# Performance work log

Measured on AMD Instinct MI355X. Metric: run time of the kernel, lower is better.

Reference implementation:

```python
import jax, jax.numpy as jnp
import numpy as np

B, L, D = 4, 4096, 256


def setup_inputs() -> dict:
    key = jax.random.key(0)
    k_x, k_q, k_k, k_v, k_w, k_b = jax.random.split(key, 6)
    s = 1.0 / np.sqrt(D)
    return {
        "x": jax.random.normal(k_x, (B, L, D), dtype=jnp.float32),
        "Wq": jax.random.normal(k_q, (D, D), dtype=jnp.float32) * s,   # nn.Linear weight (out,in)
        "Wk": jax.random.normal(k_k, (D, D), dtype=jnp.float32) * s,
        "Wv": jax.random.normal(k_v, (D, D), dtype=jnp.float32) * s,
        "w_mlp": jax.random.normal(k_w, (D,), dtype=jnp.float32) * s,  # Linear(D,1) weight
        "b_mlp": jnp.zeros((), dtype=jnp.float32),                     # Linear(D,1) bias
    }


def reference(x, Wq, Wk, Wv, w_mlp, b_mlp):
    # Projections (nn.Linear: y = x @ W.T, no bias)
    Q = jnp.einsum("bld,ed->ble", x, Wq)
    K = jnp.einsum("bld,ed->ble", x, Wk)
    V = jnp.einsum("bld,ed->ble", x, Wv)
    # score[b,i,j] = relu((Q[b,i]-K[b,j]) @ w_mlp + b_mlp)
    # decomposed: (Q-K)@w = Q@w - K@w  (exact same math, no (B,L,L,D) tensor)
    q_s = Q @ w_mlp  # (B,L)
    k_s = K @ w_mlp  # (B,L)
    scores = jax.nn.relu(q_s[:, :, None] - k_s[:, None, :] + b_mlp)  # (B,L,L)
    attn = jax.nn.softmax(scores, axis=-1)  # softmax over key axis j
    # out[b,i,d] = sum_j attn[b,i,j] * V[b,j,d]
    out = jnp.einsum("bij,bjd->bid", attn, V)
    return out  # dropout p=0.0 is identity
```

## Files before the change

kernel.cpp:

```cpp
#include <hip/hip_runtime.h>
#include <math.h>

#define BB 4
#define LL 4096
#define DD 256
#define NROWS (BB*LL)
#define CHUNK 32
#define NC (LL/CHUNK)
#define NB 8192

typedef __bf16 bf16x8 __attribute__((ext_vector_type(8)));
typedef __bf16 bf16x4 __attribute__((ext_vector_type(4)));
typedef float floatx4 __attribute__((ext_vector_type(4)));

__global__ void k_prep(const float* __restrict__ Wq, const float* __restrict__ Wk,
                       const float* __restrict__ Wv, const float* __restrict__ w,
                       float* __restrict__ u_part,
                       __bf16* __restrict__ Wh, __bf16* __restrict__ Wl) {
    __shared__ float wl[16];
    int d = threadIdx.x;
    int e0 = blockIdx.x * 16;
    if (d < 16) wl[d] = w[e0 + d];
    __syncthreads();
    float aq = 0.f, ak = 0.f;
    #pragma unroll
    for (int j = 0; j < 16; ++j) {
        float we = wl[j];
        aq = fmaf(Wq[(size_t)(e0 + j)*DD + d], we, aq);
        ak = fmaf(Wk[(size_t)(e0 + j)*DD + d], we, ak);
        float wv = Wv[(size_t)(e0 + j)*DD + d];
        __bf16 h = (__bf16)wv;
        Wh[(size_t)(e0 + j)*DD + d] = h;
        Wl[(size_t)(e0 + j)*DD + d] = (__bf16)(wv - (float)h);
    }
    u_part[(size_t)blockIdx.x*512 + d]       = aq;
    u_part[(size_t)blockIdx.x*512 + DD + d]  = ak;
}

__global__ void __launch_bounds__(256) k_gemm_mfma(
        const float* __restrict__ x,
        const __bf16* __restrict__ Wh, const __bf16* __restrict__ Wl,
        const float* __restrict__ u_part, const float* __restrict__ bmlp,
        float* __restrict__ V, float* __restrict__ a, float* __restrict__ c) {
    __shared__ __bf16 Ah[2][32*40];
    __shared__ __bf16 Al[2][32*40];
    __shared__ float4 ul[128];
    __shared__ float pros[512];
    const int tid = threadIdx.x;
    const int wave = tid >> 6, lane = tid & 63;
    const int rowBase = blockIdx.x * 32;
    const int colBase = blockIdx.y * 128;
    const int quad = lane >> 4, l16 = lane & 15;
    const int srow = tid >> 3, skq = (tid & 7) * 4;
    const bool doproj = (blockIdx.y == 0);

    if (doproj && tid < 128) {
        float4 s = make_float4(0.f, 0.f, 0.f, 0.f);
        #pragma unroll
        for (int g = 0; g < 16; ++g) {
            float4 p = *(const float4*)(u_part + (size_t)g*512 + tid*4);
            s.x += p.x; s.y += p.y; s.z += p.z; s.w += p.w;
        }
        ul[tid] = s;
    }
    __syncthreads();

    floatx4 acc[2][2];
    #pragma unroll
    for (int rt = 0; rt < 2; ++rt)
        #pragma unroll
        for (int ct = 0; ct < 2; ++ct)
            acc[rt][ct] = (floatx4){0.f, 0.f, 0.f, 0.f};
    float aq = 0.f, ak = 0.f;

    const float* xrow = x + (size_t)(rowBase + srow)*DD + skq;

    {
        float4 xv = *(const float4*)xrow;
        __bf16 h0 = (__bf16)xv.x, h1 = (__bf16)xv.y, h2 = (__bf16)xv.z, h3 = (__bf16)xv.w;
        bf16x4 hv = {h0, h1, h2, h3};
        bf16x4 lv = {(__bf16)(xv.x - (float)h0), (__bf16)(xv.y - (float)h1),
                     (__bf16)(xv.z - (float)h2), (__bf16)(xv.w - (float)h3)};
        *(bf16x4*)&Ah[0][srow*40 + skq] = hv;
        *(bf16x4*)&Al[0][srow*40 + skq] = lv;
        if (doproj) {
            float4 q4 = ul[(tid & 7)];
            float4 k4 = ul[64 + (tid & 7)];
            aq = fmaf(xv.x, q4.x, fmaf(xv.y, q4.y, fmaf(xv.z, q4.z, fmaf(xv.w, q4.w, aq))));
            ak = fmaf(xv.x, k4.x, fmaf(xv.y, k4.y, fmaf(xv.z, k4.z, fmaf(xv.w, k4.w, ak))));
        }
    }
    __syncthreads();

    for (int t = 0; t < 8; ++t) {
        const int k0 = t * 32;
        const int cur = t & 1;
        float4 xv;
        if (t < 7) xv = *(const float4*)(xrow + k0 + 32);
        bf16x8 ah[2], al[2];
        #pragma unroll
        for (int rt = 0; rt < 2; ++rt) {
            int m = rt*16 + l16;
            ah[rt] = *(bf16x8*)&Ah[cur][m*40 + quad*8];
            al[rt] = *(bf16x8*)&Al[cur][m*40 + quad*8];
        }
        if (t < 7) {
            __bf16 h0 = (__bf16)xv.x, h1 = (__bf16)xv.y, h2 = (__bf16)xv.z, h3 = (__bf16)xv.w;
            bf16x4 hv = {h0, h1, h2, h3};
            bf16x4 lv = {(__bf16)(xv.x - (float)h0), (__bf16)(xv.y - (float)h1),
                         (__bf16)(xv.z - (float)h2), (__bf16)(xv.w - (float)h3)};
            *(bf16x4*)&Ah[cur^1][srow*40 + skq] = hv;
            *(bf16x4*)&Al[cur^1][srow*40 + skq] = lv;
            if (doproj) {
                float4 q4 = ul[((k0 + 32) >> 2) + (tid & 7)];
                float4 k4 = ul[64 + ((k0 + 32) >> 2) + (tid & 7)];
                aq = fmaf(xv.x, q4.x, fmaf(xv.y, q4.y, fmaf(xv.z, q4.z, fmaf(xv.w, q4.w, aq))));
                ak = fmaf(xv.x, k4.x, fmaf(xv.y, k4.y, fmaf(xv.z, k4.z, fmaf(xv.w, k4.w, ak))));
            }
        }
        __syncthreads();
        #pragma unroll
        for (int ct = 0; ct < 2; ++ct) {
            int n = colBase + wave*32 + ct*16 + l16;
            bf16x8 bh = *(const bf16x8*)(Wh + (size_t)n*DD + k0 + quad*8);
            bf16x8 bl = *(const bf16x8*)(Wl + (size_t)n*DD + k0 + quad*8);
            #pragma unroll
            for (int rt = 0; rt < 2; ++rt) {
                acc[rt][ct] = __builtin_amdgcn_mfma_f32_16x16x32_bf16(ah[rt], bh, acc[rt][ct], 0, 0, 0);
                acc[rt][ct] = __builtin_amdgcn_mfma_f32_16x16x32_bf16(ah[rt], bl, acc[rt][ct], 0, 0, 0);
                acc[rt][ct] = __builtin_amdgcn_mfma_f32_16x16x32_bf16(al[rt], bh, acc[rt][ct], 0, 0, 0);
            }
        }
    }
    #pragma unroll
    for (int rt = 0; rt < 2; ++rt)
        #pragma unroll
        for (int ct = 0; ct < 2; ++ct)
            #pragma unroll
            for (int i = 0; i < 4; ++i) {
                int row = rowBase + rt*16 + quad*4 + i;
                int col = colBase + wave*32 + ct*16 + l16;
                V[(size_t)row*DD + col] = acc[rt][ct][i];
            }
    if (doproj) {
        __syncthreads();
        pros[tid] = aq;
        pros[256 + tid] = ak;
        __syncthreads();
        if (tid < 32) {
            float sa = 0.f, sc = 0.f;
            #pragma unroll
            for (int j = 0; j < 8; ++j) {
                sa += pros[tid*8 + j];
                sc += pros[256 + tid*8 + j];
            }
            a[rowBase + tid] = sa + bmlp[0];
            c[rowBase + tid] = sc;
        }
    }
}

__global__ void __launch_bounds__(1024) k_sortish(const float* __restrict__ c,
        const float* __restrict__ a,
        int* __restrict__ perm,
        float* __restrict__ c_sorted, float* __restrict__ e_sorted,
        float* __restrict__ SE, float* __restrict__ hdr,
        float4* __restrict__ rowrec, int* __restrict__ rbs_g) {
    __shared__ int   hist[NB];
    __shared__ float esl[LL];
    __shared__ float scrf[64];
    __shared__ int   qhist[132];
    __shared__ int   rbs[132];
    int b = blockIdx.x, tid = threadIdx.x;
    int wave = tid >> 6, lane = tid & 63;
    int* scri = (int*)scrf;

    float4 cv = ((const float4*)(c + (size_t)b*LL))[tid];
    float cw[4] = {cv.x, cv.y, cv.z, cv.w};
    float mn = fminf(fminf(cw[0],cw[1]), fminf(cw[2],cw[3]));
    float mx = fmaxf(fmaxf(cw[0],cw[1]), fmaxf(cw[2],cw[3]));
    #pragma unroll
    for (int off = 32; off > 0; off >>= 1) {
        mn = fminf(mn, __shfl_down(mn, off));
        mx = fmaxf(mx, __shfl_down(mx, off));
    }
    if (lane == 0) { scrf[wave] = mn; scrf[32 + wave] = mx; }
    __syncthreads();
    if (wave == 0) {
        float m = (lane < 16) ? scrf[lane]      :  3.4e38f;
        float M = (lane < 16) ? scrf[32 + lane] : -3.4e38f;
        #pragma unroll
        for (int off = 32; off > 0; off >>= 1) {
            m = fminf(m, __shfl_down(m, off));
            M = fmaxf(M, __shfl_down(M, off));
        }
        if (lane == 0) { scrf[0] = m; scrf[1] = M; }
    }
    __syncthreads();
    float cmin = scrf[0], cmax = scrf[1];
    float scale = (float)NB / fmaxf(cmax - cmin, 1e-20f);
    __syncthreads();

    ((int4*)hist)[tid] = make_int4(0,0,0,0);
    ((int4*)hist)[tid + 1024] = make_int4(0,0,0,0);
    if (tid < 132) qhist[tid] = 0;
    __syncthreads();

    int bins[4];
    #pragma unroll
    for (int u = 0; u < 4; ++u) {
        int bi = (int)((cw[u] - cmin) * scale);
        bi = bi < 0 ? 0 : (bi > NB-1 ? NB-1 : bi);
        bins[u] = bi;
        atomicAdd(&hist[bi], 1);
    }
    __syncthreads();

    int loc[8]; int base = 0;
    #pragma unroll
    for (int j = 0; j < 8; ++j) { loc[j] = base; base += hist[tid*8 + j]; }
    int incl = base;
    #pragma unroll
    for (int off = 1; off < 64; off <<= 1) {
        int t = __shfl_up(incl, off);
        if (lane >= off) incl += t;
    }
    if (lane == 63) scri[wave] = incl;
    __syncthreads();
    if (wave == 0) {
        int v = (lane < 16) ? scri[lane] : 0;
        int s = v;
        #pragma unroll
        for (int off = 1; off < 16; off <<= 1) {
            int t = __shfl_up(s, off);
            if (lane >= off) s += t;
        }
        if (lane < 16) scri[lane] = s - v;
    }
    __syncthreads();
    int thread_excl = (incl - base) + scri[wave];
    __syncthreads();
    #pragma unroll
    for (int j = 0; j < 8; ++j) {
        int bs = thread_excl + loc[j];
        hist[tid*8 + j] = bs;
    }
    if (tid == 0) {
        hdr[b*2 + 0] = cmin;
        hdr[b*2 + 1] = scale;
    }
    __syncthreads();

    float4 av = ((const float4*)(a + (size_t)b*LL))[tid];
    float aw[4] = {av.x, av.y, av.z, av.w};
    int qq[4]; float4 rec[4];
    #pragma unroll
    for (int u = 0; u < 4; ++u) {
        float t = (aw[u] - cmin) * scale;
        int ibb = t < 0.f ? 0 : (t >= (float)NB ? NB : (int)t);
        int k   = (ibb == NB)     ? LL : hist[ibb];
        int ke  = (ibb >= NB - 1) ? LL : hist[ibb + 1];
        qq[u] = k >> 5;
        rec[u] = make_float4(aw[u], __int_as_float(k), __int_as_float(ke),
                             __int_as_float(tid*4 + u));
        atomicAdd(&qhist[qq[u]], 1);
    }
    __syncthreads();

    #pragma unroll
    for (int u = 0; u < 4; ++u) {
        int i = tid*4 + u;
        int r = atomicAdd(&hist[bins[u]], 1);
        float e = expf(cmin - cw[u]);
        perm[(size_t)b*LL + r] = i;
        c_sorted[(size_t)b*LL + r] = cw[u];
        e_sorted[(size_t)b*LL + r] = e;
        esl[r] = e;
    }
    __syncthreads();

    if (wave == 0) {
        int v0 = qhist[2*lane], v1 = qhist[2*lane+1];
        int ps = v0 + v1;
        int qi = ps;
        #pragma unroll
        for (int off = 1; off < 64; off <<= 1) {
            int tu = __shfl_up(qi, off);
            if (lane >= off) qi += tu;
        }
        rbs[2*lane]     = qi - ps;
        rbs[2*lane + 1] = qi - v1;
        if (lane == 63) { rbs[128] = qi; rbs[129] = qi + qhist[128]; }
    }
    __syncthreads();
    if (tid < 129) qhist[tid] = rbs[tid];
    if (tid < 130) rbs_g[b*130 + tid] = rbs[tid];
    __syncthreads();
    #pragma unroll
    for (int u = 0; u < 4; ++u) {
        int r = atomicAdd(&qhist[qq[u]], 1);
        rowrec[(size_t)b*LL + r] = rec[u];
    }

    float le[4]; float s0 = 0.f;
    #pragma unroll
    for (int u = 0; u < 4; ++u) { le[u] = s0; s0 += esl[tid*4 + u]; }
    float fincl = s0;
    #pragma unroll
    for (int off = 1; off < 64; off <<= 1) {
        float t = __shfl_up(fincl, off);
        if (lane >= off) fincl += t;
    }
    if (lane == 63) scrf[wave] = fincl;
    __syncthreads();
    if (wave == 0) {
        float v = (lane < 16) ? scrf[lane] : 0.f;
        float s = v;
        #pragma unroll
        for (int off = 1; off < 16; off <<= 1) {
            float t = __shfl_up(s, off);
            if (lane >= off) s += t;
        }
        if (lane < 16) scrf[lane] = s - v;
    }
    __syncthreads();
    float texcl = (fincl - s0) + scrf[wave];
    #pragma unroll
    for (int u = 0; u < 4; ++u)
        SE[(size_t)b*(LL+1) + tid*4 + u] = texcl + le[u];
    if (tid == 1023) SE[(size_t)b*(LL+1) + LL] = texcl + s0;
}

__device__ __forceinline__ void chunk_out_phase(
    int b, int q, int tid, const float (&vr)[CHUNK], const float* ev_l,
    float* Plds, float* Pelds,
    float* bp_l, float* be_l, float* pt_l, float* pe_l,
    const float* __restrict__ baseP, const float* __restrict__ basePe,
    const float4* __restrict__ rowrec, const int* __restrict__ rbs_g,
    const float* __restrict__ SE, const float* __restrict__ hdr,
    const float* __restrict__ c_sorted, const float* __restrict__ e_sorted,
    const int* __restrict__ perm, const float* __restrict__ V,
    float* __restrict__ out)
{
    {
        size_t o  = ((size_t)b*(NC+1) + q)*DD + tid;
        size_t ot = ((size_t)b*(NC+1) + NC)*DD + tid;
        bp_l[tid] = baseP[o];  be_l[tid] = basePe[o];
        pt_l[tid] = baseP[ot]; pe_l[tid] = basePe[ot];
    }
    float accp = 0.f, acce = 0.f;
    #pragma unroll
    for (int r = 0; r < CHUNK; ++r) {
        Plds[r*DD + tid] = accp; Pelds[r*DD + tid] = acce;
        accp += vr[r]; acce = fmaf(ev_l[r], vr[r], acce);
    }
    Plds[CHUNK*DD + tid] = accp; Pelds[CHUNK*DD + tid] = acce;
    __syncthreads();
    const int wave = tid >> 6, lane = tid & 63;
    const int db = lane * 4;
    const float cmin = hdr[b*2];
    const float4 bp4 = *(const float4*)&bp_l[db];
    const float4 be4 = *(const float4*)&be_l[db];
    const float4 pt4 = *(const float4*)&pt_l[db];
    const int rs = rbs_g[b*130 + q];
    const int re = rbs_g[b*130 + q + ((q == NC-1) ? 2 : 1)];
    for (int t = rs + wave; t < re; t += 4) {
        float4 rr = rowrec[(size_t)b*LL + t];
        float ai = rr.x;
        int k    = __float_as_int(rr.y);
        int kend = __float_as_int(rr.z);
        int i    = __float_as_int(rr.w);
        float alpha = expf(cmin - ai);
        int local = k - q*CHUNK;
        const float4 pl4 = *(const float4*)&Plds[local*DD + db];
        const float4 pe4 = *(const float4*)&Pelds[local*DD + db];
        float Z = fmaf(alpha, (float)(LL - k), SE[(size_t)b*(LL+1) + k]);
        float4 num;
        num.x = fmaf(alpha, pt4.x - (pl4.x + bp4.x), pe4.x + be4.x);
        num.y = fmaf(alpha, pt4.y - (pl4.y + bp4.y), pe4.y + be4.y);
        num.z = fmaf(alpha, pt4.z - (pl4.z + bp4.z), pe4.z + be4.z);
        num.w = fmaf(alpha, pt4.w - (pl4.w + bp4.w), pe4.w + be4.w);
        for (int r = k; r < kend; ++r) {
            float cr = c_sorted[(size_t)b*LL + r];
            if (cr < ai) {
                float w = e_sorted[(size_t)b*LL + r] - alpha;
                int j = perm[(size_t)b*LL + r];
                float4 v = *(const float4*)(V + ((size_t)b*LL + j)*DD + db);
                num.x = fmaf(w, v.x, num.x);
                num.y = fmaf(w, v.y, num.y);
                num.z = fmaf(w, v.z, num.z);
                num.w = fmaf(w, v.w, num.w);
                Z += w;
            }
        }
        float invZ = 1.f / Z;
        float4 o;
        o.x = num.x * invZ; o.y = num.y * invZ; o.z = num.z * invZ; o.w = num.w * invZ;
        *(float4*)(out + ((size_t)b*LL + i)*DD + db) = o;
    }
}

__global__ void __launch_bounds__(256) k_tot(
    const float* __restrict__ V, const int* __restrict__ perm,
    const float* __restrict__ e_sorted,
    float* __restrict__ Tp, float* __restrict__ Te)
{
    __shared__ float ev_l[CHUNK];
    __shared__ int   pj_l[CHUNK];
    const int q = blockIdx.x, b = blockIdx.y, tid = threadIdx.x;
    if (tid < CHUNK) {
        pj_l[tid] = perm[(size_t)b*LL + q*CHUNK + tid];
        ev_l[tid] = e_sorted[(size_t)b*LL + q*CHUNK + tid];
    }
    __syncthreads();
    float sp = 0.f, se = 0.f;
    #pragma unroll
    for (int r = 0; r < CHUNK; ++r) {
        float v = V[((size_t)b*LL + pj_l[r])*DD + tid];
        sp += v; se = fmaf(ev_l[r], v, se);
    }
    Tp[((size_t)b*NC + q)*DD + tid] = sp;
    Te[((size_t)b*NC + q)*DD + tid] = se;
}

__global__ void k_base(const float* __restrict__ Tp, const float* __restrict__ Te,
        float* __restrict__ baseP, float* __restrict__ basePe) {
    int q = blockIdx.x, b = blockIdx.y, d = threadIdx.x;
    float acc = 0.f, acce = 0.f;
    #pragma unroll 8
    for (int i = 0; i < q; ++i) {
        size_t ti = ((size_t)b*NC + i) * DD + d;
        acc += Tp[ti]; acce += Te[ti];
    }
    size_t o = ((size_t)b*(NC+1) + q) * DD + d;
    baseP[o] = acc; basePe[o] = acce;
}

__global__ void __launch_bounds__(256, 2) k_outf(
    const float* __restrict__ V, const int* __restrict__ perm,
    const float* __restrict__ e_sorted, const float* __restrict__ c_sorted,
    const float4* __restrict__ rowrec, const int* __restrict__ rbs_g,
    const float* __restrict__ SE, const float* __restrict__ hdr,
    const float* __restrict__ baseP, const float* __restrict__ basePe,
    float* __restrict__ out)
{
    __shared__ float Plds[(CHUNK+1)*DD];
    __shared__ float Pelds[(CHUNK+1)*DD];
    __shared__ float bp_l[DD], be_l[DD], pt_l[DD], pe_l[DD];
    __shared__ float ev_l[CHUNK];
    __shared__ int   pj_l[CHUNK];
    const int q = blockIdx.x, b = blockIdx.y, tid = threadIdx.x;
    if (tid < CHUNK) {
        pj_l[tid] = perm[(size_t)b*LL + q*CHUNK + tid];
        ev_l[tid] = e_sorted[(size_t)b*LL + q*CHUNK + tid];
    }
    __syncthreads();
    float vr[CHUNK];
    #pragma unroll
    for (int r = 0; r < CHUNK; ++r)
        vr[r] = V[((size_t)b*LL + pj_l[r])*DD + tid];
    chunk_out_phase(b, q, tid, vr, ev_l, Plds, Pelds, bp_l, be_l, pt_l, pe_l,
                    baseP, basePe, rowrec, rbs_g, SE, hdr,
                    c_sorted, e_sorted, perm, V, out);
}

extern "C" void kernel_launch(void* const* d_in, const int* in_sizes, int n_in,
                              void* d_out, int out_size, void* d_ws, size_t ws_size,
                              hipStream_t stream) {
    const float* x  = (const float*)d_in[0];
    const float* Wq = (const float*)d_in[1];
    const float* Wk = (const float*)d_in[2];
    const float* Wv = (const float*)d_in[3];
    const float* wm = (const float*)d_in[4];
    const float* bm = (const float*)d_in[5];
    float* out = (float*)d_out;
    float* ws = (float*)d_ws;

    size_t off = 0;
    auto alloc = [&](size_t n) {
        float* p = ws + off;
        off += (n + 255) & ~(size_t)255;
        return p;
    };
    float* u_part   = alloc(16*512);
    float* a        = alloc(NROWS);
    float* c        = alloc(NROWS);
    float* c_sorted = alloc(NROWS);
    float* e_sorted = alloc(NROWS);
    float* SE       = alloc((size_t)BB*(LL+1));
    int*   perm     = (int*)alloc(NROWS);
    float* hdr      = alloc(2*BB);
    float* V        = alloc((size_t)NROWS*DD);
    float* Tp       = alloc((size_t)BB*NC*DD);
    float* Te       = alloc((size_t)BB*NC*DD);
    float* baseP    = alloc((size_t)BB*(NC+1)*DD);
    float* basePe   = alloc((size_t)BB*(NC+1)*DD);
    float4* rowrec  = (float4*)alloc((size_t)NROWS*4);
    int*   rbs_g    = (int*)alloc(BB*130);
    __bf16* Wh      = (__bf16*)alloc((size_t)DD*DD/2);
    __bf16* Wl      = (__bf16*)alloc((size_t)DD*DD/2);

    hipLaunchKernelGGL(k_prep, dim3(16), dim3(DD), 0, stream, Wq, Wk, Wv, wm, u_part, Wh, Wl);
    hipLaunchKernelGGL(k_gemm_mfma, dim3(NROWS/32, 2), dim3(256), 0, stream,
                       x, Wh, Wl, u_part, bm, V, a, c);
    hipLaunchKernelGGL(k_sortish, dim3(BB), dim3(1024), 0, stream,
                       c, a, perm, c_sorted, e_sorted, SE, hdr, rowrec, rbs_g);
    hipLaunchKernelGGL(k_tot, dim3(NC, BB), dim3(256), 0, stream,
                       V, perm, e_sorted, Tp, Te);
    hipLaunchKernelGGL(k_base, dim3(NC+1, BB), dim3(256), 0, stream,
                       Tp, Te, baseP, basePe);
    hipLaunchKernelGGL(k_outf, dim3(NC, BB), dim3(256), 0, stream,
                       V, perm, e_sorted, c_sorted, rowrec, rbs_g,
                       SE, hdr, baseP, basePe, out);
}
```

Measured before the change: 140.9 us.

## Widen GEMM tile to full D and fold chunk-prefix kernel into output kernel

The GEMM kernel now computes all 256 output columns per 32-row block instead of splitting columns across two blocks. This halves the grid, removes the duplicated x loads and bf16 split work, and lets every block compute the a/c projections. The separate k_base prefix-sum kernel is removed. k_outf instead sums the per-chunk totals Tp/Te itself to get its exclusive prefix and the grand total, which drops one launch and the baseP/basePe round trip. The cost is more accumulator registers in the GEMM, less parallelism there, and each output block reading all NC chunk totals.

```diff
diff --git a/kernel.cpp b/kernel.cpp
--- a/kernel.cpp
+++ b/kernel.cpp
@@ -49,12 +49,10 @@
     const int tid = threadIdx.x;
     const int wave = tid >> 6, lane = tid & 63;
     const int rowBase = blockIdx.x * 32;
-    const int colBase = blockIdx.y * 128;
     const int quad = lane >> 4, l16 = lane & 15;
     const int srow = tid >> 3, skq = (tid & 7) * 4;
-    const bool doproj = (blockIdx.y == 0);
-
-    if (doproj && tid < 128) {
+
+    if (tid < 128) {
         float4 s = make_float4(0.f, 0.f, 0.f, 0.f);
         #pragma unroll
         for (int g = 0; g < 16; ++g) {
@@ -65,11 +63,11 @@
     }
     __syncthreads();
 
-    floatx4 acc[2][2];
+    floatx4 acc[2][4];
     #pragma unroll
     for (int rt = 0; rt < 2; ++rt)
         #pragma unroll
-        for (int ct = 0; ct < 2; ++ct)
+        for (int ct = 0; ct < 4; ++ct)
             acc[rt][ct] = (floatx4){0.f, 0.f, 0.f, 0.f};
     float aq = 0.f, ak = 0.f;
 
@@ -83,12 +81,10 @@
                      (__bf16)(xv.z - (float)h2), (__bf16)(xv.w - (float)h3)};
         *(bf16x4*)&Ah[0][srow*40 + skq] = hv;
         *(bf16x4*)&Al[0][srow*40 + skq] = lv;
-        if (doproj) {
-            float4 q4 = ul[(tid & 7)];
-            float4 k4 = ul[64 + (tid & 7)];
-            aq = fmaf(xv.x, q4.x, fmaf(xv.y, q4.y, fmaf(xv.z, q4.z, fmaf(xv.w, q4.w, aq))));
-            ak = fmaf(xv.x, k4.x, fmaf(xv.y, k4.y, fmaf(xv.z, k4.z, fmaf(xv.w, k4.w, ak))));
-        }
+        float4 q4 = ul[(tid & 7)];
+        float4 k4 = ul[64 + (tid & 7)];
+        aq = fmaf(xv.x, q4.x, fmaf(xv.y, q4.y, fmaf(xv.z, q4.z, fmaf(xv.w, q4.w, aq))));
+        ak = fmaf(xv.x, k4.x, fmaf(xv.y, k4.y, fmaf(xv.z, k4.z, fmaf(xv.w, k4.w, ak))));
     }
     __syncthreads();
 
@@ -111,17 +107,15 @@
                          (__bf16)(xv.z - (float)h2), (__bf16)(xv.w - (float)h3)};
             *(bf16x4*)&Ah[cur^1][srow*40 + skq] = hv;
             *(bf16x4*)&Al[cur^1][srow*40 + skq] = lv;
-            if (doproj) {
-                float4 q4 = ul[((k0 + 32) >> 2) + (tid & 7)];
-                float4 k4 = ul[64 + ((k0 + 32) >> 2) + (tid & 7)];
-                aq = fmaf(xv.x, q4.x, fmaf(xv.y, q4.y, fmaf(xv.z, q4.z, fmaf(xv.w, q4.w, aq))));
-                ak = fmaf(xv.x, k4.x, fmaf(xv.y, k4.y, fmaf(xv.z, k4.z, fmaf(xv.w, k4.w, ak))));
-            }
+            float4 q4 = ul[((k0 + 32) >> 2) + (tid & 7)];
+            float4 k4 = ul[64 + ((k0 + 32) >> 2) + (tid & 7)];
+            aq = fmaf(xv.x, q4.x, fmaf(xv.y, q4.y, fmaf(xv.z, q4.z, fmaf(xv.w, q4.w, aq))));
+            ak = fmaf(xv.x, k4.x, fmaf(xv.y, k4.y, fmaf(xv.z, k4.z, fmaf(xv.w, k4.w, ak))));
         }
         __syncthreads();
         #pragma unroll
-        for (int ct = 0; ct < 2; ++ct) {
-            int n = colBase + wave*32 + ct*16 + l16;
+        for (int ct = 0; ct < 4; ++ct) {
+            int n = wave*64 + ct*16 + l16;
             bf16x8 bh = *(const bf16x8*)(Wh + (size_t)n*DD + k0 + quad*8);
             bf16x8 bl = *(const bf16x8*)(Wl + (size_t)n*DD + k0 + quad*8);
             #pragma unroll
@@ -135,14 +129,14 @@
     #pragma unroll
     for (int rt = 0; rt < 2; ++rt)
         #pragma unroll
-        for (int ct = 0; ct < 2; ++ct)
+        for (int ct = 0; ct < 4; ++ct)
             #pragma unroll
             for (int i = 0; i < 4; ++i) {
                 int row = rowBase + rt*16 + quad*4 + i;
-                int col = colBase + wave*32 + ct*16 + l16;
+                int col = wave*64 + ct*16 + l16;
                 V[(size_t)row*DD + col] = acc[rt][ct][i];
             }
-    if (doproj) {
+    {
         __syncthreads();
         pros[tid] = aq;
         pros[256 + tid] = ak;
@@ -331,23 +325,61 @@
     if (tid == 1023) SE[(size_t)b*(LL+1) + LL] = texcl + s0;
 }
 
-__device__ __forceinline__ void chunk_out_phase(
-    int b, int q, int tid, const float (&vr)[CHUNK], const float* ev_l,
-    float* Plds, float* Pelds,
-    float* bp_l, float* be_l, float* pt_l, float* pe_l,
-    const float* __restrict__ baseP, const float* __restrict__ basePe,
+__global__ void __launch_bounds__(256) k_tot(
+    const float* __restrict__ V, const int* __restrict__ perm,
+    const float* __restrict__ e_sorted,
+    float* __restrict__ Tp, float* __restrict__ Te)
+{
+    __shared__ float ev_l[CHUNK];
+    __shared__ int   pj_l[CHUNK];
+    const int q = blockIdx.x, b = blockIdx.y, tid = threadIdx.x;
+    if (tid < CHUNK) {
+        pj_l[tid] = perm[(size_t)b*LL + q*CHUNK + tid];
+        ev_l[tid] = e_sorted[(size_t)b*LL + q*CHUNK + tid];
+    }
+    __syncthreads();
+    float sp = 0.f, se = 0.f;
+    #pragma unroll
+    for (int r = 0; r < CHUNK; ++r) {
+        float v = V[((size_t)b*LL + pj_l[r])*DD + tid];
+        sp += v; se = fmaf(ev_l[r], v, se);
+    }
+    Tp[((size_t)b*NC + q)*DD + tid] = sp;
+    Te[((size_t)b*NC + q)*DD + tid] = se;
+}
+
+__global__ void __launch_bounds__(256, 2) k_outf(
+    const float* __restrict__ V, const int* __restrict__ perm,
+    const float* __restrict__ e_sorted, const float* __restrict__ c_sorted,
     const float4* __restrict__ rowrec, const int* __restrict__ rbs_g,
     const float* __restrict__ SE, const float* __restrict__ hdr,
-    const float* __restrict__ c_sorted, const float* __restrict__ e_sorted,
-    const int* __restrict__ perm, const float* __restrict__ V,
+    const float* __restrict__ Tp, const float* __restrict__ Te,
     float* __restrict__ out)
 {
-    {
-        size_t o  = ((size_t)b*(NC+1) + q)*DD + tid;
-        size_t ot = ((size_t)b*(NC+1) + NC)*DD + tid;
-        bp_l[tid] = baseP[o];  be_l[tid] = basePe[o];
-        pt_l[tid] = baseP[ot]; pe_l[tid] = basePe[ot];
-    }
+    __shared__ float Plds[(CHUNK+1)*DD];
+    __shared__ float Pelds[(CHUNK+1)*DD];
+    __shared__ float bp_l[DD], be_l[DD], pt_l[DD];
+    __shared__ float ev_l[CHUNK];
+    __shared__ int   pj_l[CHUNK];
+    const int q = blockIdx.x, b = blockIdx.y, tid = threadIdx.x;
+    if (tid < CHUNK) {
+        pj_l[tid] = perm[(size_t)b*LL + q*CHUNK + tid];
+        ev_l[tid] = e_sorted[(size_t)b*LL + q*CHUNK + tid];
+    }
+    __syncthreads();
+    float vr[CHUNK];
+    #pragma unroll
+    for (int r = 0; r < CHUNK; ++r)
+        vr[r] = V[((size_t)b*LL + pj_l[r])*DD + tid];
+    float bp = 0.f, be = 0.f, pt = 0.f;
+    #pragma unroll 8
+    for (int i = 0; i < NC; ++i) {
+        float tp = Tp[((size_t)b*NC + i)*DD + tid];
+        float te = Te[((size_t)b*NC + i)*DD + tid];
+        if (i < q) { bp += tp; be += te; }
+        pt += tp;
+    }
+    bp_l[tid] = bp; be_l[tid] = be; pt_l[tid] = pt;
     float accp = 0.f, acce = 0.f;
     #pragma unroll
     for (int r = 0; r < CHUNK; ++r) {
@@ -400,70 +432,6 @@
     }
 }
 
-__global__ void __launch_bounds__(256) k_tot(
-    const float* __restrict__ V, const int* __restrict__ perm,
-    const float* __restrict__ e_sorted,
-    float* __restrict__ Tp, float* __restrict__ Te)
-{
-    __shared__ float ev_l[CHUNK];
-    __shared__ int   pj_l[CHUNK];
-    const int q = blockIdx.x, b = blockIdx.y, tid = threadIdx.x;
-    if (tid < CHUNK) {
-        pj_l[tid] = perm[(size_t)b*LL + q*CHUNK + tid];
-        ev_l[tid] = e_sorted[(size_t)b*LL + q*CHUNK + tid];
-    }
-    __syncthreads();
-    float sp = 0.f, se = 0.f;
-    #pragma unroll
-    for (int r = 0; r < CHUNK; ++r) {
-        float v = V[((size_t)b*LL + pj_l[r])*DD + tid];
-        sp += v; se = fmaf(ev_l[r], v, se);
-    }
-    Tp[((size_t)b*NC + q)*DD + tid] = sp;
-    Te[((size_t)b*NC + q)*DD + tid] = se;
-}
-
-__global__ void k_base(const float* __restrict__ Tp, const float* __restrict__ Te,
-        float* __restrict__ baseP, float* __restrict__ basePe) {
-    int q = blockIdx.x, b = blockIdx.y, d = threadIdx.x;
-    float acc = 0.f, acce = 0.f;
-    #pragma unroll 8
-    for (int i = 0; i < q; ++i) {
-        size_t ti = ((size_t)b*NC + i) * DD + d;
-        acc += Tp[ti]; acce += Te[ti];
-    }
-    size_t o = ((size_t)b*(NC+1) + q) * DD + d;
-    baseP[o] = acc; basePe[o] = acce;
-}
-
-__global__ void __launch_bounds__(256, 2) k_outf(
-    const float* __restrict__ V, const int* __restrict__ perm,
-    const float* __restrict__ e_sorted, const float* __restrict__ c_sorted,
-    const float4* __restrict__ rowrec, const int* __restrict__ rbs_g,
-    const float* __restrict__ SE, const float* __restrict__ hdr,
-    const float* __restrict__ baseP, const float* __restrict__ basePe,
-    float* __restrict__ out)
-{
-    __shared__ float Plds[(CHUNK+1)*DD];
-    __shared__ float Pelds[(CHUNK+1)*DD];
-    __shared__ float bp_l[DD], be_l[DD], pt_l[DD], pe_l[DD];
-    __shared__ float ev_l[CHUNK];
-    __shared__ int   pj_l[CHUNK];
-    const int q = blockIdx.x, b = blockIdx.y, tid = threadIdx.x;
-    if (tid < CHUNK) {
-        pj_l[tid] = perm[(size_t)b*LL + q*CHUNK + tid];
-        ev_l[tid] = e_sorted[(size_t)b*LL + q*CHUNK + tid];
-    }
-    __syncthreads();
-    float vr[CHUNK];
-    #pragma unroll
-    for (int r = 0; r < CHUNK; ++r)
-        vr[r] = V[((size_t)b*LL + pj_l[r])*DD + tid];
-    chunk_out_phase(b, q, tid, vr, ev_l, Plds, Pelds, bp_l, be_l, pt_l, pe_l,
-                    baseP, basePe, rowrec, rbs_g, SE, hdr,
-                    c_sorted, e_sorted, perm, V, out);
-}
-
 extern "C" void kernel_launch(void* const* d_in, const int* in_sizes, int n_in,
                               void* d_out, int out_size, void* d_ws, size_t ws_size,
                               hipStream_t stream) {
@@ -493,23 +461,19 @@
     float* V        = alloc((size_t)NROWS*DD);
     float* Tp       = alloc((size_t)BB*NC*DD);
     float* Te       = alloc((size_t)BB*NC*DD);
-    float* baseP    = alloc((size_t)BB*(NC+1)*DD);
-    float* basePe   = alloc((size_t)BB*(NC+1)*DD);
     float4* rowrec  = (float4*)alloc((size_t)NROWS*4);
     int*   rbs_g    = (int*)alloc(BB*130);
     __bf16* Wh      = (__bf16*)alloc((size_t)DD*DD/2);
     __bf16* Wl      = (__bf16*)alloc((size_t)DD*DD/2);
 
     hipLaunchKernelGGL(k_prep, dim3(16), dim3(DD), 0, stream, Wq, Wk, Wv, wm, u_part, Wh, Wl);
-    hipLaunchKernelGGL(k_gemm_mfma, dim3(NROWS/32, 2), dim3(256), 0, stream,
+    hipLaunchKernelGGL(k_gemm_mfma, dim3(NROWS/32), dim3(256), 0, stream,
                        x, Wh, Wl, u_part, bm, V, a, c);
     hipLaunchKernelGGL(k_sortish, dim3(BB), dim3(1024), 0, stream,
                        c, a, perm, c_sorted, e_sorted, SE, hdr, rowrec, rbs_g);
     hipLaunchKernelGGL(k_tot, dim3(NC, BB), dim3(256), 0, stream,
                        V, perm, e_sorted, Tp, Te);
-    hipLaunchKernelGGL(k_base, dim3(NC+1, BB), dim3(256), 0, stream,
-                       Tp, Te, baseP, basePe);
     hipLaunchKernelGGL(k_outf, dim3(NC, BB), dim3(256), 0, stream,
                        V, perm, e_sorted, c_sorted, rowrec, rbs_g,
-                       SE, hdr, baseP, basePe, out);
-}
+                       SE, hdr, Tp, Te, out);
+}
```

After: 157.3 us. 1.12x slower.

## Replace LDS prefix tables with per-row register prefix and split rows across blocks

Applied to the files above, without the earlier changes.

The output kernel no longer builds per-chunk prefix sums of V in shared memory. Each thread keeps its column's chunk values in registers and recomputes the predicated prefix for each query row. Rows of a chunk are also split across two blocks via a z grid dimension. This cuts the large LDS footprint and a barrier to raise occupancy and parallelism, at the cost of redundant V gathers per split and extra ALU work per row.

```diff
diff --git a/kernel.cpp b/kernel.cpp
--- a/kernel.cpp
+++ b/kernel.cpp
@@ -8,6 +8,7 @@
 #define CHUNK 32
 #define NC (LL/CHUNK)
 #define NB 8192
+#define SPLIT 2
 
 typedef __bf16 bf16x8 __attribute__((ext_vector_type(8)));
 typedef __bf16 bf16x4 __attribute__((ext_vector_type(4)));
@@ -331,75 +332,6 @@
     if (tid == 1023) SE[(size_t)b*(LL+1) + LL] = texcl + s0;
 }
 
-__device__ __forceinline__ void chunk_out_phase(
-    int b, int q, int tid, const float (&vr)[CHUNK], const float* ev_l,
-    float* Plds, float* Pelds,
-    float* bp_l, float* be_l, float* pt_l, float* pe_l,
-    const float* __restrict__ baseP, const float* __restrict__ basePe,
-    const float4* __restrict__ rowrec, const int* __restrict__ rbs_g,
-    const float* __restrict__ SE, const float* __restrict__ hdr,
-    const float* __restrict__ c_sorted, const float* __restrict__ e_sorted,
-    const int* __restrict__ perm, const float* __restrict__ V,
-    float* __restrict__ out)
-{
-    {
-        size_t o  = ((size_t)b*(NC+1) + q)*DD + tid;
-        size_t ot = ((size_t)b*(NC+1) + NC)*DD + tid;
-        bp_l[tid] = baseP[o];  be_l[tid] = basePe[o];
-        pt_l[tid] = baseP[ot]; pe_l[tid] = basePe[ot];
-    }
-    float accp = 0.f, acce = 0.f;
-    #pragma unroll
-    for (int r = 0; r < CHUNK; ++r) {
-        Plds[r*DD + tid] = accp; Pelds[r*DD + tid] = acce;
-        accp += vr[r]; acce = fmaf(ev_l[r], vr[r], acce);
-    }
-    Plds[CHUNK*DD + tid] = accp; Pelds[CHUNK*DD + tid] = acce;
-    __syncthreads();
-    const int wave = tid >> 6, lane = tid & 63;
-    const int db = lane * 4;
-    const float cmin = hdr[b*2];
-    const float4 bp4 = *(const float4*)&bp_l[db];
-    const float4 be4 = *(const float4*)&be_l[db];
-    const float4 pt4 = *(const float4*)&pt_l[db];
-    const int rs = rbs_g[b*130 + q];
-    const int re = rbs_g[b*130 + q + ((q == NC-1) ? 2 : 1)];
-    for (int t = rs + wave; t < re; t += 4) {
-        float4 rr = rowrec[(size_t)b*LL + t];
-        float ai = rr.x;
-        int k    = __float_as_int(rr.y);
-        int kend = __float_as_int(rr.z);
-        int i    = __float_as_int(rr.w);
-        float alpha = expf(cmin - ai);
-        int local = k - q*CHUNK;
-        const float4 pl4 = *(const float4*)&Plds[local*DD + db];
-        const float4 pe4 = *(const float4*)&Pelds[local*DD + db];
-        float Z = fmaf(alpha, (float)(LL - k), SE[(size_t)b*(LL+1) + k]);
-        float4 num;
-        num.x = fmaf(alpha, pt4.x - (pl4.x + bp4.x), pe4.x + be4.x);
-        num.y = fmaf(alpha, pt4.y - (pl4.y + bp4.y), pe4.y + be4.y);
-        num.z = fmaf(alpha, pt4.z - (pl4.z + bp4.z), pe4.z + be4.z);
-        num.w = fmaf(alpha, pt4.w - (pl4.w + bp4.w), pe4.w + be4.w);
-        for (int r = k; r < kend; ++r) {
-            float cr = c_sorted[(size_t)b*LL + r];
-            if (cr < ai) {
-                float w = e_sorted[(size_t)b*LL + r] - alpha;
-                int j = perm[(size_t)b*LL + r];
-                float4 v = *(const float4*)(V + ((size_t)b*LL + j)*DD + db);
-                num.x = fmaf(w, v.x, num.x);
-                num.y = fmaf(w, v.y, num.y);
-                num.z = fmaf(w, v.z, num.z);
-                num.w = fmaf(w, v.w, num.w);
-                Z += w;
-            }
-        }
-        float invZ = 1.f / Z;
-        float4 o;
-        o.x = num.x * invZ; o.y = num.y * invZ; o.z = num.z * invZ; o.w = num.w * invZ;
-        *(float4*)(out + ((size_t)b*LL + i)*DD + db) = o;
-    }
-}
-
 __global__ void __launch_bounds__(256) k_tot(
     const float* __restrict__ V, const int* __restrict__ perm,
     const float* __restrict__ e_sorted,
@@ -436,7 +368,7 @@
     baseP[o] = acc; basePe[o] = acce;
 }
 
-__global__ void __launch_bounds__(256, 2) k_outf(
+__global__ void __launch_bounds__(256) k_outr(
     const float* __restrict__ V, const int* __restrict__ perm,
     const float* __restrict__ e_sorted, const float* __restrict__ c_sorted,
     const float4* __restrict__ rowrec, const int* __restrict__ rbs_g,
@@ -444,24 +376,60 @@
     const float* __restrict__ baseP, const float* __restrict__ basePe,
     float* __restrict__ out)
 {
-    __shared__ float Plds[(CHUNK+1)*DD];
-    __shared__ float Pelds[(CHUNK+1)*DD];
-    __shared__ float bp_l[DD], be_l[DD], pt_l[DD], pe_l[DD];
     __shared__ float ev_l[CHUNK];
     __shared__ int   pj_l[CHUNK];
-    const int q = blockIdx.x, b = blockIdx.y, tid = threadIdx.x;
+    const int q = blockIdx.x, b = blockIdx.y, z = blockIdx.z;
+    const int tid = threadIdx.x;
+    const int rs = rbs_g[b*130 + q];
+    const int re = rbs_g[b*130 + q + ((q == NC-1) ? 2 : 1)];
+    if (rs + z >= re) return;
     if (tid < CHUNK) {
         pj_l[tid] = perm[(size_t)b*LL + q*CHUNK + tid];
         ev_l[tid] = e_sorted[(size_t)b*LL + q*CHUNK + tid];
     }
     __syncthreads();
-    float vr[CHUNK];
+    float vr[CHUNK], evr[CHUNK];
     #pragma unroll
     for (int r = 0; r < CHUNK; ++r)
         vr[r] = V[((size_t)b*LL + pj_l[r])*DD + tid];
-    chunk_out_phase(b, q, tid, vr, ev_l, Plds, Pelds, bp_l, be_l, pt_l, pe_l,
-                    baseP, basePe, rowrec, rbs_g, SE, hdr,
-                    c_sorted, e_sorted, perm, V, out);
+    #pragma unroll
+    for (int r = 0; r < CHUNK; ++r)
+        evr[r] = ev_l[r];
+    const float cmin = hdr[b*2];
+    const float bp = baseP [((size_t)b*(NC+1) + q )*DD + tid];
+    const float be = basePe[((size_t)b*(NC+1) + q )*DD + tid];
+    const float pt = baseP [((size_t)b*(NC+1) + NC)*DD + tid];
+    for (int t = rs + z; t < re; t += SPLIT) {
+        float4 rr = rowrec[(size_t)b*LL + t];
+        float ai = rr.x;
+        int k    = __float_as_int(rr.y);
+        int kend = __float_as_int(rr.z);
+        int i    = __float_as_int(rr.w);
+        float alpha = expf(cmin - ai);
+        int local = k - q*CHUNK;
+        float pl = 0.f, pe = 0.f;
+        #pragma unroll
+        for (int r = 0; r < CHUNK; ++r) {
+            float npl = pl + vr[r];
+            float npe = fmaf(evr[r], vr[r], pe);
+            pl = (r < local) ? npl : pl;
+            pe = (r < local) ? npe : pe;
+        }
+        float Z = fmaf(alpha, (float)(LL - k), SE[(size_t)b*(LL+1) + k]);
+        float num = fmaf(alpha, pt - (pl + bp), pe + be);
+        for (int r = k; r < kend; ++r) {
+            float cr = c_sorted[(size_t)b*LL + r];
+            if (cr < ai) {
+                float w = e_sorted[(size_t)b*LL + r] - alpha;
+                int j = perm[(size_t)b*LL + r];
+                float v = V[((size_t)b*LL + j)*DD + tid];
+                num = fmaf(w, v, num);
+                Z += w;
+            }
+        }
+        float invZ = 1.f / Z;
+        out[((size_t)b*LL + i)*DD + tid] = num * invZ;
+    }
 }
 
 extern "C" void kernel_launch(void* const* d_in, const int* in_sizes, int n_in,
@@ -509,7 +477,7 @@
                        V, perm, e_sorted, Tp, Te);
     hipLaunchKernelGGL(k_base, dim3(NC+1, BB), dim3(256), 0, stream,
                        Tp, Te, baseP, basePe);
-    hipLaunchKernelGGL(k_outf, dim3(NC, BB), dim3(256), 0, stream,
+    hipLaunchKernelGGL(k_outr, dim3(NC, BB, SPLIT), dim3(256), 0, stream,
                        V, perm, e_sorted, c_sorted, rowrec, rbs_g,
                        SE, hdr, baseP, basePe, out);
 }
```

Result: slower. 163.7 us (+16.2%).
